# Optimization experiments

Measured on AMD Instinct MI355X. Metric: run time of the kernel, lower is better.

The kernel has to match this reference:

```python
import jax, jax.numpy as jnp
import numpy as np


def _glorot(key, shape):
    fan_in, fan_out = shape[0], shape[1]
    lim = np.sqrt(6.0 / (fan_in + fan_out))
    return jax.random.uniform(key, shape, jnp.float32, -lim, lim)


def setup_inputs() -> dict:
    key = jax.random.key(0)
    ks = jax.random.split(key, 32)
    B, NR, NT = 16384, 64, 128
    inp = {
        "tier0_features": jax.random.normal(ks[0], (B, 44), jnp.float32),
        "robot_features": jax.random.normal(ks[1], (B, NR, 6), jnp.float32),
        "track_features": jax.random.normal(ks[2], (B, NT, 7), jnp.float32),
        # robot SetEncoder: 6 -> 64 -> 64 -> 32
        "rw1": _glorot(ks[3], (6, 64)),  "rb1": jnp.zeros((64,), jnp.float32),
        "rw2": _glorot(ks[4], (64, 64)), "rb2": jnp.zeros((64,), jnp.float32),
        "rw3": _glorot(ks[5], (64, 32)), "rb3": jnp.zeros((32,), jnp.float32),
        # track SetEncoder: 7 -> 64 -> 64 -> 32
        "tw1": _glorot(ks[6], (7, 64)),  "tb1": jnp.zeros((64,), jnp.float32),
        "tw2": _glorot(ks[7], (64, 64)), "tb2": jnp.zeros((64,), jnp.float32),
        "tw3": _glorot(ks[8], (64, 32)), "tb3": jnp.zeros((32,), jnp.float32),
        # head MLP: 108 -> 128 -> 128 -> 64 -> 1
        "mw1": _glorot(ks[9], (108, 128)),  "mb1": jnp.zeros((128,), jnp.float32),
        "mw2": _glorot(ks[10], (128, 128)), "mb2": jnp.zeros((128,), jnp.float32),
        "mw3": _glorot(ks[11], (128, 64)),  "mb3": jnp.zeros((64,), jnp.float32),
        "mw4": _glorot(ks[12], (64, 1)),    "mb4": jnp.zeros((1,), jnp.float32),
    }
    return inp


def _set_encode(x, w1, b1, w2, b2, w3, b3):
    # x: [B, N, d_in] -> pooled [B, 32]; mask=None path: mean+max over set dim
    h = jax.nn.relu(jnp.einsum('bnd,dh->bnh', x, w1) + b1)
    h = jax.nn.relu(jnp.einsum('bnh,hk->bnk', h, w2) + b2)
    e = jnp.einsum('bnk,ko->bno', h, w3) + b3
    return (e.mean(axis=1) + e.max(axis=1)) * 0.5


def reference(tier0_features, robot_features, track_features,
              rw1, rb1, rw2, rb2, rw3, rb3,
              tw1, tb1, tw2, tb2, tw3, tb3,
              mw1, mb1, mw2, mb2, mw3, mb3, mw4, mb4):
    robot_emb = _set_encode(robot_features, rw1, rb1, rw2, rb2, rw3, rb3)  # [B,32]
    track_emb = _set_encode(track_features, tw1, tb1, tw2, tb2, tw3, tb3)  # [B,32]
    c = jnp.concatenate([tier0_features, robot_emb, track_emb], axis=1)    # [B,108]
    h = jax.nn.relu(c @ mw1 + mb1)
    h = jax.nn.relu(h @ mw2 + mb2)
    h = jax.nn.relu(h @ mw3 + mb3)
    return (h @ mw4 + mb4).squeeze(-1)  # [B]
```

## Files before the change

### kernel.cpp

```cpp
#include <hip/hip_runtime.h>
#include <hip/hip_bf16.h>

#define DEV_INLINE __device__ __forceinline__

typedef __bf16 bf16x8 __attribute__((ext_vector_type(8)));
typedef float  floatx4 __attribute__((ext_vector_type(4)));

DEV_INLINE bf16x8 ld_frag(const __bf16* p) {
    union { uint4 u; bf16x8 v; } t;
    t.u = *(const uint4*)p;
    return t.v;
}
DEV_INLINE bf16x8 pack_relu2(floatx4 a, floatx4 b) {
    float2 p0 = {fmaxf(a[0], 0.0f), fmaxf(a[1], 0.0f)};
    float2 p1 = {fmaxf(a[2], 0.0f), fmaxf(a[3], 0.0f)};
    float2 p2 = {fmaxf(b[0], 0.0f), fmaxf(b[1], 0.0f)};
    float2 p3 = {fmaxf(b[2], 0.0f), fmaxf(b[3], 0.0f)};
    union { __hip_bfloat162 h[4]; bf16x8 v; } t;
    t.h[0] = __float22bfloat162_rn(p0);
    t.h[1] = __float22bfloat162_rn(p1);
    t.h[2] = __float22bfloat162_rn(p2);
    t.h[3] = __float22bfloat162_rn(p3);
    return t.v;
}
DEV_INLINE floatx4 vmax4(floatx4 a, floatx4 b) {
    floatx4 r;
#pragma unroll
    for (int i = 0; i < 4; ++i) r[i] = fmaxf(a[i], b[i]);
    return r;
}

template<int N, int Kp, int Ks>
DEV_INLINE void tp(__bf16* dst, const float* __restrict__ src, int idx0, int stride) {
    for (int e = idx0; e < N * Kp; e += stride) {
        int n = e / Kp, k = e - n * Kp;
        dst[e] = (k < Ks) ? (__bf16)src[k * N + n] : (__bf16)0.0f;
    }
}
template<int N, int K>
DEV_INLINE void tp_perm(__bf16* dst, const float* __restrict__ src, int idx0, int stride) {
    for (int e = idx0; e < N * K; e += stride) {
        int n = e / K, kh = e - n * K;
        int qd = (kh >> 3) & 3, kq = kh >> 5, j = kh & 7;
        int c = (2 * kq + (j >> 2)) * 16 + qd * 4 + (j & 3);
        dst[e] = (__bf16)src[c * N + n];
    }
}

__global__ __launch_bounds__(256)
void prep_kernel(const float* __restrict__ rw1, const float* __restrict__ rw2,
                 const float* __restrict__ rw3,
                 const float* __restrict__ tw1, const float* __restrict__ tw2,
                 const float* __restrict__ tw3,
                 const float* __restrict__ mw1, const float* __restrict__ mw2,
                 const float* __restrict__ mw3, __bf16* __restrict__ wb)
{
    int i0 = blockIdx.x * 256 + threadIdx.x;
    int st = gridDim.x * 256;
    tp     < 64,  32,   6>(wb + 0,     rw1, i0, st);
    tp_perm< 64,  64>     (wb + 2048,  rw2, i0, st);
    tp_perm< 32,  64>     (wb + 6144,  rw3, i0, st);
    tp     < 64,  32,   7>(wb + 8192,  tw1, i0, st);
    tp_perm< 64,  64>     (wb + 10240, tw2, i0, st);
    tp_perm< 32,  64>     (wb + 14336, tw3, i0, st);
    tp     <128, 128, 108>(wb + 16384, mw1, i0, st);
    tp_perm<128, 128>     (wb + 32768, mw2, i0, st);
    tp_perm< 64, 128>     (wb + 49152, mw3, i0, st);
}

struct __align__(16) EncSmem {
    float e3s[64 * 36];
    float e3m[64 * 36];
    float pool[512];
    float bs[160];
};

template<int DIN, int S, int ITERS>
DEV_INLINE void enc_loop(EncSmem& sm, const float* __restrict__ X,
                         const __bf16* __restrict__ w1p,
                         const __bf16* __restrict__ w2p,
                         const __bf16* __restrict__ w3p,
                         const float* __restrict__ b1, const float* __restrict__ b2,
                         const float* __restrict__ b3,
                         __bf16* __restrict__ out, int bid0)
{
    constexpr int NB = 128 / S;
    const int tid = threadIdx.x;
    const int w   = tid >> 6;
    const int l64 = tid & 63;
    const int ln  = l64 & 15;
    const int qd  = l64 >> 4;

    if (tid < 160)
        sm.bs[tid] = (tid < 64) ? b1[tid]
                   : (tid < 128) ? b2[tid - 64] : b3[tid - 128];

    bf16x8 w1f[4], w2f[4][2], w3f[2][2];
#pragma unroll
    for (int mt = 0; mt < 4; ++mt)
        w1f[mt] = ld_frag(&w1p[(mt * 16 + ln) * 32 + qd * 8]);
#pragma unroll
    for (int mt = 0; mt < 4; ++mt)
#pragma unroll
        for (int kq = 0; kq < 2; ++kq)
            w2f[mt][kq] = ld_frag(&w2p[(mt * 16 + ln) * 64 + kq * 32 + qd * 8]);
#pragma unroll
    for (int mt = 0; mt < 2; ++mt)
#pragma unroll
        for (int kq = 0; kq < 2; ++kq)
            w3f[mt][kq] = ld_frag(&w3p[(mt * 16 + ln) * 64 + kq * 32 + qd * 8]);
    __syncthreads();

    for (int it = 0; it < ITERS; ++it) {
        const int bid = bid0 + it;

        bf16x8 xb[2];
#pragma unroll
        for (int t = 0; t < 2; ++t) {
            bf16x8 v;
#pragma unroll
            for (int j = 0; j < 8; ++j) v[j] = (__bf16)0.0f;
            if (qd == 0) {
                const int row = (2 * w + t) * 16 + ln;
                const float* xp = X + ((size_t)bid * 128 + row) * DIN;
#pragma unroll
                for (int j = 0; j < DIN; ++j) v[j] = (__bf16)xp[j];
            }
            xb[t] = v;
        }
        floatx4 a1[2][4];
#pragma unroll
        for (int mt = 0; mt < 4; ++mt) {
            float4 bv = *(const float4*)&sm.bs[mt * 16 + qd * 4];
#pragma unroll
            for (int t = 0; t < 2; ++t) {
                floatx4 acc = (floatx4){bv.x, bv.y, bv.z, bv.w};
                a1[t][mt] = __builtin_amdgcn_mfma_f32_16x16x32_bf16(w1f[mt], xb[t], acc, 0, 0, 0);
            }
        }
        bf16x8 f1[2][2];
#pragma unroll
        for (int t = 0; t < 2; ++t)
#pragma unroll
            for (int kq = 0; kq < 2; ++kq)
                f1[t][kq] = pack_relu2(a1[t][2 * kq], a1[t][2 * kq + 1]);

        floatx4 a2[2][4];
#pragma unroll
        for (int mt = 0; mt < 4; ++mt) {
            float4 bv = *(const float4*)&sm.bs[64 + mt * 16 + qd * 4];
#pragma unroll
            for (int t = 0; t < 2; ++t) {
                floatx4 acc = (floatx4){bv.x, bv.y, bv.z, bv.w};
                acc = __builtin_amdgcn_mfma_f32_16x16x32_bf16(w2f[mt][0], f1[t][0], acc, 0, 0, 0);
                acc = __builtin_amdgcn_mfma_f32_16x16x32_bf16(w2f[mt][1], f1[t][1], acc, 0, 0, 0);
                a2[t][mt] = acc;
            }
        }
        bf16x8 f2[2][2];
#pragma unroll
        for (int t = 0; t < 2; ++t)
#pragma unroll
            for (int kq = 0; kq < 2; ++kq)
                f2[t][kq] = pack_relu2(a2[t][2 * kq], a2[t][2 * kq + 1]);

        floatx4 a3[2][2];
#pragma unroll
        for (int mt = 0; mt < 2; ++mt) {
            float4 bv = *(const float4*)&sm.bs[128 + mt * 16 + qd * 4];
#pragma unroll
            for (int t = 0; t < 2; ++t) {
                floatx4 acc = (floatx4){bv.x, bv.y, bv.z, bv.w};
                acc = __builtin_amdgcn_mfma_f32_16x16x32_bf16(w3f[mt][0], f2[t][0], acc, 0, 0, 0);
                acc = __builtin_amdgcn_mfma_f32_16x16x32_bf16(w3f[mt][1], f2[t][1], acc, 0, 0, 0);
                a3[t][mt] = acc;
            }
        }
#pragma unroll
        for (int mt = 0; mt < 2; ++mt) {
            floatx4 s = a3[0][mt] + a3[1][mt];
            floatx4 m = vmax4(a3[0][mt], a3[1][mt]);
            float4 so = {s[0], s[1], s[2], s[3]};
            float4 mo = {m[0], m[1], m[2], m[3]};
            *(float4*)&sm.e3s[(w * 16 + ln) * 36 + mt * 16 + qd * 4] = so;
            *(float4*)&sm.e3m[(w * 16 + ln) * 36 + mt * 16 + qd * 4] = mo;
        }
        __syncthreads();

        {
            constexpr int R = 64 / NB;
            const int o  = tid & 31;
            const int bi = (tid >> 5) % NB;
            const int ch = tid / (32 * NB);
            const int p0 = bi * R + ch * 8;
            float s = 0.0f, m = -3.4e38f;
#pragma unroll
            for (int r = 0; r < 8; ++r) {
                s += sm.e3s[(p0 + r) * 36 + o];
                m = fmaxf(m, sm.e3m[(p0 + r) * 36 + o]);
            }
            sm.pool[tid] = s;
            sm.pool[256 + tid] = m;
        }
        __syncthreads();
        if (tid < NB * 32) {
            constexpr int C = 8 / NB;
            float s = 0.0f, m = -3.4e38f;
#pragma unroll
            for (int c = 0; c < C; ++c) {
                s += sm.pool[tid + c * 32 * NB];
                m = fmaxf(m, sm.pool[256 + tid + c * 32 * NB]);
            }
            size_t b = (size_t)bid * NB + (tid >> 5);
            out[b * 32 + (tid & 31)] = (__bf16)(0.5f * (s * (1.0f / S) + m));
        }
    }
}

__global__ __launch_bounds__(256, 3)
void enc_fused(const float* __restrict__ rX, const float* __restrict__ tX,
               const __bf16* __restrict__ wb,
               const float* __restrict__ rb1, const float* __restrict__ rb2,
               const float* __restrict__ rb3,
               const float* __restrict__ tb1, const float* __restrict__ tb2,
               const float* __restrict__ tb3,
               __bf16* __restrict__ remb, __bf16* __restrict__ temb)
{
    __shared__ EncSmem sm;
    if ((int)blockIdx.x < 256)
        enc_loop<6, 64, 32>(sm, rX, wb, wb + 2048, wb + 6144,
                            rb1, rb2, rb3, remb, blockIdx.x * 32);
    else
        enc_loop<7, 128, 32>(sm, tX, wb + 8192, wb + 10240, wb + 14336,
                             tb1, tb2, tb3, temb, (blockIdx.x - 256) * 32);
}

__global__ __launch_bounds__(256)
void head_mfma(const float* __restrict__ t0,
               const __bf16* __restrict__ remb, const __bf16* __restrict__ temb,
               const __bf16* __restrict__ hw1, const float* __restrict__ b1,
               const __bf16* __restrict__ hw2, const float* __restrict__ b2,
               const __bf16* __restrict__ hw3, const float* __restrict__ b3,
               const float* __restrict__ w4, const float* __restrict__ b4,
               float* __restrict__ out)
{
    __shared__ __align__(16) __bf16 cb[64 * 136];

    const int tid = threadIdx.x;
    const int w   = tid >> 6;
    const int l64 = tid & 63;
    const int ln  = l64 & 15;
    const int qd  = l64 >> 4;
    const int g0  = blockIdx.x * 64;

    for (int i = tid; i < 64 * 44; i += 256) {
        int r = i / 44, k = i - r * 44;
        cb[r * 136 + k] = (__bf16)t0[(size_t)(g0 + r) * 44 + k];
    }
    for (int i = tid; i < 64 * 32; i += 256) {
        int r = i >> 5, k = i & 31;
        cb[r * 136 + 44 + k] = remb[(size_t)(g0 + r) * 32 + k];
        cb[r * 136 + 76 + k] = temb[(size_t)(g0 + r) * 32 + k];
    }
    for (int i = tid; i < 64 * 20; i += 256) {
        int r = i / 20, k = i - r * 20;
        cb[r * 136 + 108 + k] = (__bf16)0.0f;
    }
    __syncthreads();

    bf16x8 cf[4];
#pragma unroll
    for (int kq = 0; kq < 4; ++kq)
        cf[kq] = ld_frag(&cb[(w * 16 + ln) * 136 + kq * 32 + qd * 8]);
    floatx4 acc1[8];
#pragma unroll
    for (int mt = 0; mt < 8; ++mt) {
        float4 bv = *(const float4*)&b1[mt * 16 + qd * 4];
        floatx4 acc = (floatx4){bv.x, bv.y, bv.z, bv.w};
#pragma unroll
        for (int kq = 0; kq < 4; ++kq) {
            bf16x8 af = ld_frag(&hw1[(mt * 16 + ln) * 128 + kq * 32 + qd * 8]);
            acc = __builtin_amdgcn_mfma_f32_16x16x32_bf16(af, cf[kq], acc, 0, 0, 0);
        }
        acc1[mt] = acc;
    }
    bf16x8 f1[4];
#pragma unroll
    for (int kq = 0; kq < 4; ++kq)
        f1[kq] = pack_relu2(acc1[2 * kq], acc1[2 * kq + 1]);

    floatx4 acc2[8];
#pragma unroll
    for (int mt = 0; mt < 8; ++mt) {
        float4 bv = *(const float4*)&b2[mt * 16 + qd * 4];
        floatx4 acc = (floatx4){bv.x, bv.y, bv.z, bv.w};
#pragma unroll
        for (int kq = 0; kq < 4; ++kq) {
            bf16x8 af = ld_frag(&hw2[(mt * 16 + ln) * 128 + kq * 32 + qd * 8]);
            acc = __builtin_amdgcn_mfma_f32_16x16x32_bf16(af, f1[kq], acc, 0, 0, 0);
        }
        acc2[mt] = acc;
    }
    bf16x8 f2[4];
#pragma unroll
    for (int kq = 0; kq < 4; ++kq)
        f2[kq] = pack_relu2(acc2[2 * kq], acc2[2 * kq + 1]);

    floatx4 acc3[4];
#pragma unroll
    for (int mt = 0; mt < 4; ++mt) {
        float4 bv = *(const float4*)&b3[mt * 16 + qd * 4];
        floatx4 acc = (floatx4){bv.x, bv.y, bv.z, bv.w};
#pragma unroll
        for (int kq = 0; kq < 4; ++kq) {
            bf16x8 af = ld_frag(&hw3[(mt * 16 + ln) * 128 + kq * 32 + qd * 8]);
            acc = __builtin_amdgcn_mfma_f32_16x16x32_bf16(af, f2[kq], acc, 0, 0, 0);
        }
        acc3[mt] = acc;
    }

    float part = 0.0f;
#pragma unroll
    for (int mt = 0; mt < 4; ++mt) {
        float4 wv = *(const float4*)&w4[mt * 16 + qd * 4];
        part = fmaf(fmaxf(acc3[mt][0], 0.0f), wv.x, part);
        part = fmaf(fmaxf(acc3[mt][1], 0.0f), wv.y, part);
        part = fmaf(fmaxf(acc3[mt][2], 0.0f), wv.z, part);
        part = fmaf(fmaxf(acc3[mt][3], 0.0f), wv.w, part);
    }
    part += __shfl_xor(part, 16);
    part += __shfl_xor(part, 32);
    if (qd == 0)
        out[g0 + w * 16 + ln] = part + b4[0];
}

extern "C" void kernel_launch(void* const* d_in, const int* in_sizes, int n_in,
                              void* d_out, int out_size, void* d_ws, size_t ws_size,
                              hipStream_t stream)
{
    const float* t0  = (const float*)d_in[0];
    const float* rX  = (const float*)d_in[1];
    const float* tX  = (const float*)d_in[2];
    const float* rw1 = (const float*)d_in[3];  const float* rb1 = (const float*)d_in[4];
    const float* rw2 = (const float*)d_in[5];  const float* rb2 = (const float*)d_in[6];
    const float* rw3 = (const float*)d_in[7];  const float* rb3 = (const float*)d_in[8];
    const float* tw1 = (const float*)d_in[9];  const float* tb1 = (const float*)d_in[10];
    const float* tw2 = (const float*)d_in[11]; const float* tb2 = (const float*)d_in[12];
    const float* tw3 = (const float*)d_in[13]; const float* tb3 = (const float*)d_in[14];
    const float* mw1 = (const float*)d_in[15]; const float* mb1 = (const float*)d_in[16];
    const float* mw2 = (const float*)d_in[17]; const float* mb2 = (const float*)d_in[18];
    const float* mw3 = (const float*)d_in[19]; const float* mb3 = (const float*)d_in[20];
    const float* mw4 = (const float*)d_in[21]; const float* mb4 = (const float*)d_in[22];
    float* out = (float*)d_out;

    const int B = 16384;
    __bf16* remb = (__bf16*)d_ws;
    __bf16* temb = (__bf16*)((char*)d_ws + ((size_t)1 << 20));
    __bf16* wb   = (__bf16*)((char*)d_ws + ((size_t)2 << 20));
    const __bf16* mw1b = wb + 16384; const __bf16* mw2b = wb + 32768;
    const __bf16* mw3b = wb + 49152;

    prep_kernel<<<64, 256, 0, stream>>>(rw1, rw2, rw3, tw1, tw2, tw3,
                                        mw1, mw2, mw3, wb);
    enc_fused<<<768, 256, 0, stream>>>(rX, tX, wb,
                                       rb1, rb2, rb3, tb1, tb2, tb3,
                                       remb, temb);
    head_mfma<<<B / 64, 256, 0, stream>>>(t0, remb, temb,
                                          mw1b, mb1, mw2b, mb2, mw3b, mb3,
                                          mw4, mb4, out);
}
```

Measured before the change: 235.6 us.

## Prefetch encoder inputs into double-buffered LDS with coalesced loads, smaller tiles

The encoder now loads each 128-row input tile with coalesced per-thread loads, converts it to bf16, and stages it in a double-buffered shared-memory array. The next tile is prefetched into registers while the current one is computed. Previously one lane per row did strided scalar loads right before the MFMAs. The sum and max partials are interleaved as float2 to halve the number of LDS accesses. The grid is split into more, shorter blocks (8 iterations instead of 32) and the occupancy hint is raised to 4, so more waves can hide latency. In exchange it uses more shared memory and adds register pressure.

```diff
diff --git a/kernel.cpp b/kernel.cpp
--- a/kernel.cpp
+++ b/kernel.cpp
@@ -69,11 +69,32 @@
 }
 
 struct __align__(16) EncSmem {
-    float e3s[64 * 36];
-    float e3m[64 * 36];
-    float pool[512];
-    float bs[160];
+    float2 e3[64 * 36];
+    float2 pool[256];
+    float  bs[160];
+    __bf16 xs[2][128 * 8];
 };
+
+template<int DIN>
+DEV_INLINE void x_load(const float* __restrict__ X, int bid, int tid, float (&g)[4]) {
+    const float* src = X + (size_t)bid * 128 * DIN;
+#pragma unroll
+    for (int p = 0; p < 4; ++p) {
+        int e = tid + p * 256;
+        if ((DIN == 6) ? (p < 3) : (e < 128 * 7)) g[p] = src[e];
+    }
+}
+template<int DIN>
+DEV_INLINE void x_store(__bf16* xbuf, int tid, const float (&g)[4]) {
+#pragma unroll
+    for (int p = 0; p < 4; ++p) {
+        int e = tid + p * 256;
+        if ((DIN == 6) ? (p < 3) : (e < 128 * 7)) {
+            int r = e / DIN, k = e - r * DIN;
+            xbuf[r * 8 + k] = (__bf16)g[p];
+        }
+    }
+}
 
 template<int DIN, int S, int ITERS>
 DEV_INLINE void enc_loop(EncSmem& sm, const float* __restrict__ X,
@@ -95,6 +116,12 @@
         sm.bs[tid] = (tid < 64) ? b1[tid]
                    : (tid < 128) ? b2[tid - 64] : b3[tid - 128];
 
+    {
+        __bf16* xf = &sm.xs[0][0];
+        if (DIN == 6) *(uint32_t*)&xf[tid * 8 + 6] = 0u;
+        else          xf[tid * 8 + 7] = (__bf16)0.0f;
+    }
+
     bf16x8 w1f[4], w2f[4][2], w3f[2][2];
 #pragma unroll
     for (int mt = 0; mt < 4; ++mt)
@@ -109,10 +136,16 @@
 #pragma unroll
         for (int kq = 0; kq < 2; ++kq)
             w3f[mt][kq] = ld_frag(&w3p[(mt * 16 + ln) * 64 + kq * 32 + qd * 8]);
+
+    float g[4];
+    x_load<DIN>(X, bid0, tid, g);
+    x_store<DIN>(sm.xs[0], tid, g);
     __syncthreads();
 
+    int cur = 0;
     for (int it = 0; it < ITERS; ++it) {
         const int bid = bid0 + it;
+        if (it + 1 < ITERS) x_load<DIN>(X, bid + 1, tid, g);
 
         bf16x8 xb[2];
 #pragma unroll
@@ -122,12 +155,11 @@
             for (int j = 0; j < 8; ++j) v[j] = (__bf16)0.0f;
             if (qd == 0) {
                 const int row = (2 * w + t) * 16 + ln;
-                const float* xp = X + ((size_t)bid * 128 + row) * DIN;
-#pragma unroll
-                for (int j = 0; j < DIN; ++j) v[j] = (__bf16)xp[j];
+                v = ld_frag(&sm.xs[cur][row * 8]);
             }
             xb[t] = v;
         }
+
         floatx4 a1[2][4];
 #pragma unroll
         for (int mt = 0; mt < 4; ++mt) {
@@ -180,10 +212,11 @@
         for (int mt = 0; mt < 2; ++mt) {
             floatx4 s = a3[0][mt] + a3[1][mt];
             floatx4 m = vmax4(a3[0][mt], a3[1][mt]);
-            float4 so = {s[0], s[1], s[2], s[3]};
-            float4 mo = {m[0], m[1], m[2], m[3]};
-            *(float4*)&sm.e3s[(w * 16 + ln) * 36 + mt * 16 + qd * 4] = so;
-            *(float4*)&sm.e3m[(w * 16 + ln) * 36 + mt * 16 + qd * 4] = mo;
+            float4 lo = {s[0], m[0], s[1], m[1]};
+            float4 hi = {s[2], m[2], s[3], m[3]};
+            float2* dst = &sm.e3[(w * 16 + ln) * 36 + mt * 16 + qd * 4];
+            *(float4*)&dst[0] = lo;
+            *(float4*)&dst[2] = hi;
         }
         __syncthreads();
 
@@ -196,28 +229,32 @@
             float s = 0.0f, m = -3.4e38f;
 #pragma unroll
             for (int r = 0; r < 8; ++r) {
-                s += sm.e3s[(p0 + r) * 36 + o];
-                m = fmaxf(m, sm.e3m[(p0 + r) * 36 + o]);
-            }
-            sm.pool[tid] = s;
-            sm.pool[256 + tid] = m;
-        }
+                float2 v = sm.e3[(p0 + r) * 36 + o];
+                s += v.x;
+                m = fmaxf(m, v.y);
+            }
+            sm.pool[tid] = make_float2(s, m);
+        }
+        if (it + 1 < ITERS) x_store<DIN>(sm.xs[cur ^ 1], tid, g);
         __syncthreads();
+
         if (tid < NB * 32) {
             constexpr int C = 8 / NB;
             float s = 0.0f, m = -3.4e38f;
 #pragma unroll
             for (int c = 0; c < C; ++c) {
-                s += sm.pool[tid + c * 32 * NB];
-                m = fmaxf(m, sm.pool[256 + tid + c * 32 * NB]);
+                float2 v = sm.pool[tid + c * 32 * NB];
+                s += v.x;
+                m = fmaxf(m, v.y);
             }
             size_t b = (size_t)bid * NB + (tid >> 5);
             out[b * 32 + (tid & 31)] = (__bf16)(0.5f * (s * (1.0f / S) + m));
         }
-    }
-}
-
-__global__ __launch_bounds__(256, 3)
+        cur ^= 1;
+    }
+}
+
+__global__ __launch_bounds__(256, 4)
 void enc_fused(const float* __restrict__ rX, const float* __restrict__ tX,
                const __bf16* __restrict__ wb,
                const float* __restrict__ rb1, const float* __restrict__ rb2,
@@ -227,12 +264,12 @@
                __bf16* __restrict__ remb, __bf16* __restrict__ temb)
 {
     __shared__ EncSmem sm;
-    if ((int)blockIdx.x < 256)
-        enc_loop<6, 64, 32>(sm, rX, wb, wb + 2048, wb + 6144,
-                            rb1, rb2, rb3, remb, blockIdx.x * 32);
+    if ((int)blockIdx.x < 1024)
+        enc_loop<6, 64, 8>(sm, rX, wb, wb + 2048, wb + 6144,
+                           rb1, rb2, rb3, remb, blockIdx.x * 8);
     else
-        enc_loop<7, 128, 32>(sm, tX, wb + 8192, wb + 10240, wb + 14336,
-                             tb1, tb2, tb3, temb, (blockIdx.x - 256) * 32);
+        enc_loop<7, 128, 8>(sm, tX, wb + 8192, wb + 10240, wb + 14336,
+                            tb1, tb2, tb3, temb, ((int)blockIdx.x - 1024) * 8);
 }
 
 __global__ __launch_bounds__(256)
@@ -362,9 +399,9 @@
 
     prep_kernel<<<64, 256, 0, stream>>>(rw1, rw2, rw3, tw1, tw2, tw3,
                                         mw1, mw2, mw3, wb);
-    enc_fused<<<768, 256, 0, stream>>>(rX, tX, wb,
-                                       rb1, rb2, rb3, tb1, tb2, tb3,
-                                       remb, temb);
+    enc_fused<<<3072, 256, 0, stream>>>(rX, tX, wb,
+                                        rb1, rb2, rb3, tb1, tb2, tb3,
+                                        remb, temb);
     head_mfma<<<B / 64, 256, 0, stream>>>(t0, remb, temb,
                                           mw1b, mb1, mw2b, mb2, mw3b, mb3,
                                           mw4, mb4, out);
```

Result: faster. 221.1 us (-6.1%).
